# Kernel tuning notes

Measured on AMD Instinct MI355X. Metric: run time of the kernel, lower is better.

Reference implementation:

```python
import jax, jax.numpy as jnp
import numpy as np

LEVEL_SHAPES = ((100, 100), (50, 50), (25, 25))  # (H, W) per feature level
B, S, D, H, L, P, FFN = 2, 13125, 256, 8, 3, 4, 1024
Dh = D // H


def setup_inputs() -> dict:
    key = jax.random.key(0)
    ks = jax.random.split(key, 24)

    def rn(k, shape, s=0.02):
        return jax.random.normal(k, shape, jnp.float32) * s

    starts = np.cumsum([0] + [h * w for h, w in LEVEL_SHAPES])[:-1]
    return {
        "x": jax.random.normal(ks[0], (B, S, D), jnp.float32),
        "pos_embed": jax.random.normal(ks[1], (B, S, D), jnp.float32) * 0.1,
        "ref_points": jax.random.uniform(ks[2], (B, S, L, 2), jnp.float32),
        "W_off": rn(ks[3], (D, H * L * P * 2)),
        "b_off": rn(ks[4], (H * L * P * 2,), 0.5),
        "W_attn": rn(ks[5], (D, H * L * P)),
        "b_attn": rn(ks[6], (H * L * P,)),
        "W_val": rn(ks[7], (D, D)),
        "b_val": rn(ks[8], (D,)),
        "W_out": rn(ks[9], (D, D)),
        "b_out": rn(ks[10], (D,)),
        "g1": jnp.ones((D,), jnp.float32),
        "be1": jnp.zeros((D,), jnp.float32),
        "W1": rn(ks[11], (D, FFN)),
        "b1": rn(ks[12], (FFN,)),
        "W2": rn(ks[13], (FFN, D)),
        "b2": rn(ks[14], (D,)),
        "g2": jnp.ones((D,), jnp.float32),
        "be2": jnp.zeros((D,), jnp.float32),
        "level_shapes": jnp.array(LEVEL_SHAPES, jnp.int32),
        "level_start_idx": jnp.array(starts, jnp.int32),
    }


def layer_norm(x, g, b, eps=1e-5):
    m = jnp.mean(x, -1, keepdims=True)
    v = jnp.var(x, -1, keepdims=True)
    return (x - m) * jax.lax.rsqrt(v + eps) * g + b


def bilinear_sample(vl, loc, Hl, Wl):
    # vl: [B,H,S_l,Dh]; loc: [B,H,S,P,2] normalized (x,y) in [0,1]
    # grid_sample semantics: align_corners=False, padding_mode='zeros'
    x = loc[..., 0] * Wl - 0.5
    y = loc[..., 1] * Hl - 0.5
    x0 = jnp.floor(x)
    y0 = jnp.floor(y)
    fx = x - x0
    fy = y - y0
    x0i = x0.astype(jnp.int32)
    y0i = y0.astype(jnp.int32)
    out = 0.0
    for dy, dx, w in ((0, 0, (1 - fx) * (1 - fy)), (0, 1, fx * (1 - fy)),
                      (1, 0, (1 - fx) * fy), (1, 1, fx * fy)):
        xi = x0i + dx
        yi = y0i + dy
        valid = (xi >= 0) & (xi < Wl) & (yi >= 0) & (yi < Hl)
        idx = jnp.clip(yi, 0, Hl - 1) * Wl + jnp.clip(xi, 0, Wl - 1)
        b_, h_, s_, p_ = idx.shape
        g = jnp.take_along_axis(vl, idx.reshape(b_, h_, s_ * p_)[..., None], axis=2)
        g = g.reshape(b_, h_, s_, p_, Dh)
        out = out + g * (w * valid)[..., None]
    return out  # [B,H,S,P,Dh]


def ms_deform_attn(q, x, ref_points, W_off, b_off, W_attn, b_attn, W_val, b_val, W_out, b_out):
    value = (x @ W_val + b_val).reshape(B, S, H, Dh).transpose(0, 2, 1, 3)  # [B,H,S,Dh]
    off = (q @ W_off + b_off).reshape(B, S, H, L, P, 2)
    attn = jax.nn.softmax((q @ W_attn + b_attn).reshape(B, S, H, L * P), axis=-1)
    attn = attn.reshape(B, S, H, L, P).transpose(0, 2, 1, 3, 4)  # [B,H,S,L,P]
    # offset normalizer is (W, H) per level
    norm = jnp.array([[w, h] for h, w in LEVEL_SHAPES], jnp.float32)
    loc = ref_points[:, :, None, :, None, :] + off / norm[None, None, None, :, None, :]
    loc = loc.transpose(0, 2, 1, 3, 4, 5)  # [B,H,S,L,P,2]
    s0 = 0
    sampled = []
    for l, (Hl, Wl) in enumerate(LEVEL_SHAPES):
        vl = jax.lax.slice_in_dim(value, s0, s0 + Hl * Wl, axis=2)
        sampled.append(bilinear_sample(vl, loc[:, :, :, l], Hl, Wl))
        s0 += Hl * Wl
    sampled = jnp.stack(sampled, axis=3)  # [B,H,S,L,P,Dh]
    out = jnp.einsum('bhslp,bhslpd->bshd', attn, sampled).reshape(B, S, D)
    return out @ W_out + b_out


def reference(x, pos_embed, ref_points, W_off, b_off, W_attn, b_attn, W_val, b_val,
              W_out, b_out, g1, be1, W1, b1, W2, b2, g2, be2,
              level_shapes, level_start_idx):
    q = x + pos_embed
    attn_out = ms_deform_attn(q, x, ref_points, W_off, b_off, W_attn, b_attn,
                              W_val, b_val, W_out, b_out)
    h1 = layer_norm(x + attn_out, g1, be1)
    ffn = jax.nn.relu(h1 @ W1 + b1) @ W2 + b2
    return layer_norm(h1 + ffn, g2, be2)
```

## Files before the change

### kernel.cpp

```cpp
#include <hip/hip_runtime.h>
#include <hip/hip_bf16.h>

namespace {

constexpr int kB = 2, kS = 13125, kD = 256, kH = 8, kL = 3, kP = 4, kFFN = 1024, kDh = 32;
constexpr int kM = kB * kS;

typedef __attribute__((ext_vector_type(8))) short short8v;
typedef __attribute__((ext_vector_type(4))) float f32x4;
typedef __attribute__((ext_vector_type(2))) float f32x2;
typedef __attribute__((ext_vector_type(2))) unsigned int uint2v;

__device__ __forceinline__ float bf2f(unsigned short u) {
  unsigned int x = ((unsigned int)u) << 16;
  return __builtin_bit_cast(float, x);
}
__device__ __forceinline__ unsigned short f2bf(float f) {
  unsigned int u = __builtin_bit_cast(unsigned int, f);
  u += 0x7FFFu + ((u >> 16) & 1u);
  return (unsigned short)(u >> 16);
}

__device__ __forceinline__ void gload_lds16(const void* g, void* l) {
  __builtin_amdgcn_global_load_lds(
      (const __attribute__((address_space(1))) unsigned int*)g,
      (__attribute__((address_space(3))) unsigned int*)l, 16, 0, 0);
}

__global__ __launch_bounds__(256) void wprep_all(const float* __restrict__ Wv,
                                                 const float* __restrict__ Wo,
                                                 const float* __restrict__ Woff,
                                                 const float* __restrict__ Wattn,
                                                 const float* __restrict__ boff,
                                                 const float* __restrict__ battn,
                                                 const float* __restrict__ W1,
                                                 const float* __restrict__ W2,
                                                 unsigned short* __restrict__ Wvt,
                                                 unsigned short* __restrict__ Wot,
                                                 unsigned short* __restrict__ Wct,
                                                 float* __restrict__ bcomb,
                                                 unsigned short* __restrict__ W1t,
                                                 unsigned short* __restrict__ W2t) {
  int idx = blockIdx.x * 256 + threadIdx.x;
  if (idx < 65536) {
    int n = idx >> 8, k = idx & 255;
    Wvt[idx] = f2bf(Wv[k * 256 + n]);
  } else if (idx < 131072) {
    int j = idx - 65536;
    int n = j >> 8, k = j & 255;
    Wot[j] = f2bf(Wo[k * 256 + n]);
  } else if (idx < 204800) {
    int j = idx - 131072;
    int n = j >> 8, k = j & 255;
    int h = n / 36, jj = n - h * 36;
    float v = (jj < 24) ? Woff[(size_t)k * 192 + h * 24 + jj]
                        : Wattn[(size_t)k * 96 + h * 12 + (jj - 24)];
    Wct[j] = f2bf(v);
    if (j < 288) {
      int hh = j / 36, q = j - hh * 36;
      bcomb[j] = (q < 24) ? boff[hh * 24 + q] : battn[hh * 12 + (q - 24)];
    }
  } else if (idx < 466944) {
    int j = idx - 204800;
    int n = j >> 8, k = j & 255;
    W1t[j] = f2bf(W1[(size_t)k * 1024 + n]);
  } else if (idx < 729088) {
    int j = idx - 466944;
    int n = j >> 10, k = j & 1023;
    W2t[j] = f2bf(W2[(size_t)k * 256 + n]);
  }
}

__global__ __launch_bounds__(256) void prep_kernel(const float4* __restrict__ x,
                                                   const float4* __restrict__ pos,
                                                   ushort4* __restrict__ xb,
                                                   ushort4* __restrict__ qb, int n4) {
  int i = blockIdx.x * 256 + threadIdx.x;
  if (i < n4) {
    float4 a = x[i], b = pos[i];
    xb[i] = make_ushort4(f2bf(a.x), f2bf(a.y), f2bf(a.z), f2bf(a.w));
    qb[i] = make_ushort4(f2bf(a.x + b.x), f2bf(a.y + b.y),
                         f2bf(a.z + b.z), f2bf(a.w + b.w));
  }
}

template <int EPI, bool OBF, int MI, bool VHM>
__global__ __launch_bounds__(256) void mfma_gemm(const unsigned short* __restrict__ A,
                                                 const unsigned short* __restrict__ Bt,
                                                 const float* __restrict__ bias,
                                                 void* __restrict__ Cp,
                                                 int M, int N, int K) {
  constexpr int BM = MI * 32;
  __shared__ unsigned short smem[2 * 128 * 32];
  unsigned short* As = smem;
  unsigned short* Bs = smem + BM * 32;
  const int tid = threadIdx.x;
  const int w = tid >> 6, lane = tid & 63;
  const int m0 = blockIdx.y * BM, n0 = blockIdx.x * 128;
  const int wr = w >> 1, wc = w & 1;
  const int r_ = lane >> 2, sl = lane & 3;

  f32x4 acc[MI][4] = {};

  for (int k0 = 0; k0 < K; k0 += 32) {
#pragma unroll
    for (int i = 0; i < MI / 2; ++i) {
      const int row = i * 64 + w * 16 + r_;
      const int sg = sl ^ ((row >> 1) & 3);
      int arow = m0 + row;
      arow = arow < M ? arow : M - 1;
      gload_lds16(A + (size_t)arow * K + k0 + sg * 8, &As[(i * 64 + w * 16) * 32]);
    }
#pragma unroll
    for (int i = 0; i < 2; ++i) {
      const int row = i * 64 + w * 16 + r_;
      const int sg = sl ^ ((row >> 1) & 3);
      gload_lds16(Bt + (size_t)(n0 + row) * K + k0 + sg * 8, &Bs[(i * 64 + w * 16) * 32]);
    }
    __syncthreads();
    short8v a[MI], b[4];
#pragma unroll
    for (int mi = 0; mi < MI; ++mi) {
      const int row = wr * (MI * 16) + mi * 16 + (lane & 15);
      const int slot = (lane >> 4) ^ ((row >> 1) & 3);
      a[mi] = *(const short8v*)&As[row * 32 + slot * 8];
    }
#pragma unroll
    for (int ni = 0; ni < 4; ++ni) {
      const int row = wc * 64 + ni * 16 + (lane & 15);
      const int slot = (lane >> 4) ^ ((row >> 1) & 3);
      b[ni] = *(const short8v*)&Bs[row * 32 + slot * 8];
    }
#pragma unroll
    for (int mi = 0; mi < MI; ++mi)
#pragma unroll
      for (int ni = 0; ni < 4; ++ni)
        acc[mi][ni] = __builtin_amdgcn_mfma_f32_16x16x32_bf16(a[mi], b[ni], acc[mi][ni], 0, 0, 0);
    __syncthreads();
  }

  const int cr = lane >> 4, cc = lane & 15;
  if (OBF) {
    unsigned short* Cs = smem;
#pragma unroll
    for (int half = 0; half < MI / 2; ++half) {
      if (MI == 2 || wr == half) {
#pragma unroll
        for (int ni = 0; ni < 4; ++ni) {
          const int col = wc * 64 + ni * 16 + cc;
          const float bv = bias[n0 + col];
#pragma unroll
          for (int mi = 0; mi < MI; ++mi)
#pragma unroll
            for (int r = 0; r < 4; ++r) {
              const int loc = wr * (MI * 16) + mi * 16 + cr * 4 + r - half * 64;
              float v = acc[mi][ni][r] + bv;
              if (EPI == 2) v = fmaxf(v, 0.f);
              const int ch = (col >> 3) ^ (loc & 7);
              Cs[loc * 128 + ch * 8 + (col & 7)] = f2bf(v);
            }
        }
      }
      __syncthreads();
      const int lr = tid >> 4, lc = tid & 15;
#pragma unroll
      for (int pp = 0; pp < 4; ++pp) {
        const int loc = pp * 16 + lr;
        const int grow = m0 + half * 64 + loc;
        const short8v vv = *(const short8v*)&Cs[loc * 128 + ((lc ^ (loc & 7)) * 8)];
        if (grow < M) {
          if (VHM) {
            const int col = n0 + lc * 8;
            const int bb = grow >= kS ? 1 : 0;
            const int ss = grow - bb * kS;
            const int hh = col >> 5;
            *(short8v*)((unsigned short*)Cp +
                        (((size_t)(bb * kH + hh) * kS + ss) * kDh + (col & 31))) = vv;
          } else {
            *(short8v*)((unsigned short*)Cp + (size_t)grow * N + n0 + lc * 8) = vv;
          }
        }
      }
      __syncthreads();
    }
  } else {
#pragma unroll
    for (int ni = 0; ni < 4; ++ni) {
      const int col = n0 + wc * 64 + ni * 16 + cc;
      if (col >= N) continue;
      const float bv = bias[col];
#pragma unroll
      for (int mi = 0; mi < MI; ++mi) {
#pragma unroll
        for (int r = 0; r < 4; ++r) {
          const int row = m0 + wr * (MI * 16) + mi * 16 + cr * 4 + r;
          if (row >= M) continue;
          ((float*)Cp)[(size_t)row * N + col] = acc[mi][ni][r] + bv;
        }
      }
    }
  }
}

__global__ __launch_bounds__(512, 4) void ffn_fused(const unsigned short* __restrict__ Ain,
                                                    const unsigned short* __restrict__ W1t,
                                                    const unsigned short* __restrict__ W2t,
                                                    const float* __restrict__ b1,
                                                    const float* __restrict__ b2,
                                                    unsigned short* __restrict__ Cp,
                                                    int M) {
  __shared__ unsigned short W1s[2][64 * 256];
  __shared__ unsigned short Ps[2][2 * 64 * 32];
  const int tid = threadIdx.x;
  const int w = tid >> 6, lane = tid & 63;
  const int m0 = blockIdx.x * 64;
  const int cr = lane >> 4, cc = lane & 15;
  const int mw = w & 3;
  const int fw = w >> 2;

  short8v areg[8];
  {
    int grow = m0 + mw * 16 + cc;
    grow = grow < M ? grow : M - 1;
    const unsigned short* ap = Ain + (size_t)grow * 256 + cr * 8;
#pragma unroll
    for (int kk = 0; kk < 8; ++kk) areg[kk] = *(const short8v*)(ap + kk * 32);
  }

  auto stage_w1 = [&](int jt, int buf) {
    const unsigned short* src = W1t + (size_t)jt * 64 * 256;
#pragma unroll
    for (int it = 0; it < 4; ++it) {
      const int idx = it * 512 + tid;
      const int kk = idx >> 8;
      const int row = (idx >> 2) & 63;
      const int sl = idx & 3;
      const int ssl = sl ^ ((row >> 1) & 3);
      gload_lds16(src + (size_t)row * 256 + kk * 32 + ssl * 8, &W1s[buf][idx * 8]);
    }
  };

  f32x4 acc[4][2] = {};

  stage_w1(0, 0);
  __syncthreads();

#pragma unroll
  for (int jt = 0; jt < 16; ++jt) {
    const int buf = jt & 1;
    if (jt < 15) stage_w1(jt + 1, buf ^ 1);

    f32x4 p1[2] = {};
#pragma unroll
    for (int kk = 0; kk < 8; ++kk) {
#pragma unroll
      for (int lf = 0; lf < 2; ++lf) {
        const int row = fw * 32 + lf * 16 + cc;
        const short8v wv = *(const short8v*)
            &W1s[buf][kk * 2048 + row * 32 + ((cr ^ ((row >> 1) & 3)) * 8)];
        p1[lf] = __builtin_amdgcn_mfma_f32_16x16x32_bf16(wv, areg[kk], p1[lf], 0, 0, 0);
      }
    }
    {
      const int row = mw * 16 + cc;
      const int rsw = (row >> 1) & 3;
#pragma unroll
      for (int lf = 0; lf < 2; ++lf) {
        const float4 bv = *(const float4*)&b1[jt * 64 + fw * 32 + lf * 16 + cr * 4];
        const unsigned int u0 =
            (unsigned)f2bf(fmaxf(p1[lf][0] + bv.x, 0.f)) |
            ((unsigned)f2bf(fmaxf(p1[lf][1] + bv.y, 0.f)) << 16);
        const unsigned int u1 =
            (unsigned)f2bf(fmaxf(p1[lf][2] + bv.z, 0.f)) |
            ((unsigned)f2bf(fmaxf(p1[lf][3] + bv.w, 0.f)) << 16);
        const int slot = lf * 2 + (cr >> 1);
        uint2v* dst = (uint2v*)&Ps[buf][fw * 2048 + row * 32 + ((slot ^ rsw) * 8) + (cr & 1) * 4];
        *dst = (uint2v){u0, u1};
      }
    }

    if (jt > 0) {
      const unsigned short* Pr = Ps[buf ^ 1];
#pragma unroll
      for (int kk2 = 0; kk2 < 2; ++kk2) {
        short8v pf[4];
#pragma unroll
        for (int mi = 0; mi < 4; ++mi) {
          const int row = mi * 16 + cc;
          pf[mi] = *(const short8v*)
              &Pr[kk2 * 2048 + row * 32 + ((cr ^ ((row >> 1) & 3)) * 8)];
        }
#pragma unroll
        for (int ni = 0; ni < 2; ++ni) {
          const int ncol = w * 32 + ni * 16 + cc;
          const short8v wv = *(const short8v*)
              (W2t + (size_t)ncol * 1024 + (jt - 1) * 64 + kk2 * 32 + cr * 8);
#pragma unroll
          for (int mi = 0; mi < 4; ++mi)
            acc[mi][ni] = __builtin_amdgcn_mfma_f32_16x16x32_bf16(pf[mi], wv, acc[mi][ni], 0, 0, 0);
        }
      }
    }
    __syncthreads();
  }

  {
    const unsigned short* Pr = Ps[1];
#pragma unroll
    for (int kk2 = 0; kk2 < 2; ++kk2) {
      short8v pf[4];
#pragma unroll
      for (int mi = 0; mi < 4; ++mi) {
        const int row = mi * 16 + cc;
        pf[mi] = *(const short8v*)
            &Pr[kk2 * 2048 + row * 32 + ((cr ^ ((row >> 1) & 3)) * 8)];
      }
#pragma unroll
      for (int ni = 0; ni < 2; ++ni) {
        const int ncol = w * 32 + ni * 16 + cc;
        const short8v wv = *(const short8v*)
            (W2t + (size_t)ncol * 1024 + 15 * 64 + kk2 * 32 + cr * 8);
#pragma unroll
        for (int mi = 0; mi < 4; ++mi)
          acc[mi][ni] = __builtin_amdgcn_mfma_f32_16x16x32_bf16(pf[mi], wv, acc[mi][ni], 0, 0, 0);
      }
    }
  }
  __syncthreads();

  unsigned short* Cs = &W1s[0][0];
#pragma unroll
  for (int ni = 0; ni < 2; ++ni) {
    const int col = w * 32 + ni * 16 + cc;
    const float bv = b2[col];
#pragma unroll
    for (int mi = 0; mi < 4; ++mi)
#pragma unroll
      for (int r = 0; r < 4; ++r) {
        const int row = mi * 16 + cr * 4 + r;
        const float v = acc[mi][ni][r] + bv;
        Cs[row * 256 + (((col >> 3) ^ (row & 7)) * 8) + (col & 7)] = f2bf(v);
      }
  }
  __syncthreads();
#pragma unroll
  for (int it = 0; it < 4; ++it) {
    const int row = it * 16 + (tid >> 5);
    const int grow = m0 + row;
    const int ch = tid & 31;
    const short8v vv = *(const short8v*)&Cs[row * 256 + ((ch ^ (row & 7)) * 8)];
    if (grow < M) *(short8v*)(Cp + (size_t)grow * 256 + ch * 8) = vv;
  }
}

__device__ __forceinline__ void acc2u(f32x2* acc, unsigned u, int i, float m) {
  f32x2 v;
  v.x = __builtin_bit_cast(float, u << 16);
  v.y = __builtin_bit_cast(float, u & 0xFFFF0000u);
  acc[i] += m * v;
}
__device__ __forceinline__ void acc_corner(f32x2* acc, uint4 q, float m) {
  acc2u(acc, q.x, 0, m);
  acc2u(acc, q.y, 1, m);
  acc2u(acc, q.z, 2, m);
  acc2u(acc, q.w, 3, m);
}

__global__ __launch_bounds__(256) void sample_kernel(const unsigned short* __restrict__ value,
                                                     const float* __restrict__ oa,
                                                     const float* __restrict__ refp,
                                                     unsigned short* __restrict__ out) {
  const int tid = threadIdx.x;
  const int sub = tid >> 2;
  const int lane = tid & 3;
  const int gi = blockIdx.x * 64 + sub;
  if (gi >= kB * kS * kH) return;
  const int h = gi & 7;
  const int bs = gi >> 3;
  const int b = (bs >= kS) ? 1 : 0;

  const float* op = oa + (size_t)bs * 288 + h * 36;
  const float* al = op + 24;
  float w[12];
  float mx = -1e30f;
#pragma unroll
  for (int i = 0; i < 12; ++i) { w[i] = al[i]; mx = fmaxf(mx, w[i]); }
  float sum = 0.f;
#pragma unroll
  for (int i = 0; i < 12; ++i) { w[i] = __expf(w[i] - mx); sum += w[i]; }
  const float inv = 1.f / sum;
#pragma unroll
  for (int i = 0; i < 12; ++i) w[i] *= inv;

  const float* rp = refp + (size_t)bs * (kL * 2);
  const unsigned short* vbase = value + ((size_t)(b * kH + h) * kS) * kDh + lane * 8;

  const int LH[3] = {100, 50, 25}, LW[3] = {100, 50, 25}, LS[3] = {0, 10000, 12500};
  f32x2 acc[4] = {};
#pragma unroll
  for (int l = 0; l < 3; ++l) {
    const int Wi = LW[l], Hi = LH[l];
    const float Wl = (float)Wi, Hl = (float)Hi;
    const float rxw = rp[l * 2 + 0] * Wl - 0.5f;
    const float ryh = rp[l * 2 + 1] * Hl - 0.5f;
    const unsigned short* lvl = vbase + (size_t)LS[l] * kDh;
#pragma unroll
    for (int p = 0; p < 4; ++p) {
      const float ox = op[l * 8 + p * 2 + 0], oy = op[l * 8 + p * 2 + 1];
      const float xf = rxw + ox;
      const float yf = ryh + oy;
      const float x0f = floorf(xf), y0f = floorf(yf);
      const float fx = xf - x0f, fy = yf - y0f;
      const int x0 = (int)x0f, y0 = (int)y0f;
      const int x1 = x0 + 1, y1 = y0 + 1;
      const bool vx0 = (unsigned)x0 < (unsigned)Wi;
      const bool vx1 = (unsigned)x1 < (unsigned)Wi;
      const bool vy0 = (unsigned)y0 < (unsigned)Hi;
      const bool vy1 = (unsigned)y1 < (unsigned)Hi;
      const int cx0 = min(max(x0, 0), Wi - 1), cx1 = min(max(x1, 0), Wi - 1);
      const int cy0 = min(max(y0, 0), Hi - 1), cy1 = min(max(y1, 0), Hi - 1);
      const float aw = w[l * 4 + p];
      const float ax = aw * fx, a0 = aw - ax;
      const float w00 = a0 - a0 * fy, w10 = a0 * fy;
      const float w01 = ax - ax * fy, w11 = ax * fy;
      const float m00 = (vx0 && vy0) ? w00 : 0.f;
      const float m01 = (vx1 && vy0) ? w01 : 0.f;
      const float m10 = (vx0 && vy1) ? w10 : 0.f;
      const float m11 = (vx1 && vy1) ? w11 : 0.f;
      const int ry0 = cy0 * Wi, ry1 = cy1 * Wi;
      const uint4 q00 = *(const uint4*)(lvl + (size_t)(ry0 + cx0) * kDh);
      const uint4 q01 = *(const uint4*)(lvl + (size_t)(ry0 + cx1) * kDh);
      const uint4 q10 = *(const uint4*)(lvl + (size_t)(ry1 + cx0) * kDh);
      const uint4 q11 = *(const uint4*)(lvl + (size_t)(ry1 + cx1) * kDh);
      acc_corner(acc, q00, m00);
      acc_corner(acc, q01, m01);
      acc_corner(acc, q10, m10);
      acc_corner(acc, q11, m11);
    }
  }
  unsigned short r[8];
#pragma unroll
  for (int i = 0; i < 4; ++i) {
    r[2 * i] = f2bf(acc[i].x);
    r[2 * i + 1] = f2bf(acc[i].y);
  }
  *(short8v*)(out + (size_t)bs * kD + h * kDh + lane * 8) = *(const short8v*)r;
}

template <int WB>
__global__ __launch_bounds__(256) void lnres_kernel(const float* __restrict__ X,
                                                    const unsigned short* __restrict__ Ab,
                                                    const float* __restrict__ g,
                                                    const float* __restrict__ be,
                                                    float* __restrict__ out,
                                                    unsigned short* __restrict__ outb,
                                                    int rows) {
  const int wid = threadIdx.x >> 6, lane = threadIdx.x & 63;
  const int row = blockIdx.x * 4 + wid;
  if (row >= rows) return;
  const float4 v = ((const float4*)(X + (size_t)row * kD))[lane];
  const ushort4 a4 = ((const ushort4*)(Ab + (size_t)row * kD))[lane];
  float4 t;
  t.x = v.x + bf2f(a4.x);
  t.y = v.y + bf2f(a4.y);
  t.z = v.z + bf2f(a4.z);
  t.w = v.w + bf2f(a4.w);
  float s = t.x + t.y + t.z + t.w;
  float sq = t.x * t.x + t.y * t.y + t.z * t.z + t.w * t.w;
#pragma unroll
  for (int o = 1; o < 64; o <<= 1) {
    s += __shfl_xor(s, o);
    sq += __shfl_xor(sq, o);
  }
  const float mean = s * (1.f / kD);
  const float var = sq * (1.f / kD) - mean * mean;
  const float rs = rsqrtf(var + 1e-5f);
  const float4 gg = ((const float4*)g)[lane];
  const float4 bb = ((const float4*)be)[lane];
  float4 o4;
  o4.x = (t.x - mean) * rs * gg.x + bb.x;
  o4.y = (t.y - mean) * rs * gg.y + bb.y;
  o4.z = (t.z - mean) * rs * gg.z + bb.z;
  o4.w = (t.w - mean) * rs * gg.w + bb.w;
  ((float4*)(out + (size_t)row * kD))[lane] = o4;
  if (WB) {
    ((ushort4*)(outb + (size_t)row * kD))[lane] =
        make_ushort4(f2bf(o4.x), f2bf(o4.y), f2bf(o4.z), f2bf(o4.w));
  }
}

}

extern "C" void kernel_launch(void* const* d_in, const int* in_sizes, int n_in,
                              void* d_out, int out_size, void* d_ws, size_t ws_size,
                              hipStream_t stream) {
  const float* x      = (const float*)d_in[0];
  const float* pos    = (const float*)d_in[1];
  const float* refp   = (const float*)d_in[2];
  const float* W_off  = (const float*)d_in[3];
  const float* b_off  = (const float*)d_in[4];
  const float* W_attn = (const float*)d_in[5];
  const float* b_attn = (const float*)d_in[6];
  const float* W_val  = (const float*)d_in[7];
  const float* b_val  = (const float*)d_in[8];
  const float* W_out  = (const float*)d_in[9];
  const float* b_out  = (const float*)d_in[10];
  const float* g1     = (const float*)d_in[11];
  const float* be1    = (const float*)d_in[12];
  const float* W1     = (const float*)d_in[13];
  const float* b1     = (const float*)d_in[14];
  const float* W2     = (const float*)d_in[15];
  const float* b2     = (const float*)d_in[16];
  const float* g2     = (const float*)d_in[17];
  const float* be2    = (const float*)d_in[18];
  float* outp = (float*)d_out;

  char* ws = (char*)d_ws;
  unsigned short* Wvt = (unsigned short*)(ws + 0);
  unsigned short* Wot = (unsigned short*)(ws + 131072);
  unsigned short* Wct = (unsigned short*)(ws + 262144);
  float* bcomb        = (float*)(ws + 262144 + 288 * 512);
  unsigned short* W1t = (unsigned short*)(ws + 458752);
  unsigned short* W2t = (unsigned short*)(ws + 983040);
  const size_t MDb = (size_t)kM * kD * 2;
  char* regA = ws + 1507328;
  char* regB = regA + MDb;
  char* regC = regB + MDb;
  char* regG = regC + 43680000;

  unsigned short* xb    = (unsigned short*)regA;
  unsigned short* aob   = (unsigned short*)regA;
  unsigned short* qb    = (unsigned short*)regB;
  unsigned short* f2b   = (unsigned short*)regB;
  unsigned short* value = (unsigned short*)regC;
  float* oa   = (float*)(regC + MDb);
  float* h1   = (float*)regC;
  unsigned short* h1b = (unsigned short*)(regC + (size_t)kM * kD * 4);
  unsigned short* sv  = (unsigned short*)regG;

  const dim3 blk(256);
  const int mt64 = (kM + 63) / 64;
  const int n4 = kM * kD / 4;

  wprep_all<<<(729088 + 255) / 256, blk, 0, stream>>>(W_val, W_out, W_off, W_attn,
                                                      b_off, b_attn, W1, W2,
                                                      Wvt, Wot, Wct, bcomb, W1t, W2t);
  prep_kernel<<<(n4 + 255) / 256, blk, 0, stream>>>((const float4*)x, (const float4*)pos,
                                                    (ushort4*)xb, (ushort4*)qb, n4);
  mfma_gemm<0, true, 2, true><<<dim3(2, mt64), blk, 0, stream>>>(xb, Wvt, b_val, value,
                                                                 kM, 256, 256);
  mfma_gemm<0, false, 2, false><<<dim3(3, mt64), blk, 0, stream>>>(qb, Wct, bcomb, oa,
                                                                   kM, 288, 256);
  sample_kernel<<<(kB * kS * kH + 63) / 64, blk, 0, stream>>>(value, oa, refp, sv);
  mfma_gemm<0, true, 2, false><<<dim3(2, mt64), blk, 0, stream>>>(sv, Wot, b_out, aob,
                                                                  kM, 256, 256);
  lnres_kernel<1><<<(kM + 3) / 4, blk, 0, stream>>>(x, aob, g1, be1, h1, h1b, kM);
  ffn_fused<<<mt64, dim3(512), 0, stream>>>(h1b, W1t, W2t, b1, b2, f2b, kM);
  lnres_kernel<0><<<(kM + 3) / 4, blk, 0, stream>>>(h1, f2b, g2, be2, outp, nullptr, kM);
}
```

Before: 197.2 us.

## Restructure fused FFN: single P buffer, shared W1 fragment across two row tiles

The fused FFN kernel now has each wave compute a 16-column hidden slice for two 16-row tiles, so every W1 fragment read from LDS feeds two MFMAs. The ReLU'd hidden tile goes into a single 64x64 LDS buffer with a new XOR swizzle, and the second GEMM runs in the same iteration instead of one step behind. This halves LDS reads of W1 and shrinks the P buffer. In exchange it adds a second __syncthreads per iteration, drops the full unroll of the outer loop, and doubles the register-held A fragments.

```diff
diff --git a/kernel.cpp b/kernel.cpp
--- a/kernel.cpp
+++ b/kernel.cpp
@@ -210,21 +210,22 @@
                                                     unsigned short* __restrict__ Cp,
                                                     int M) {
   __shared__ unsigned short W1s[2][64 * 256];
-  __shared__ unsigned short Ps[2][2 * 64 * 32];
+  __shared__ unsigned short Ps[64 * 64];
   const int tid = threadIdx.x;
   const int w = tid >> 6, lane = tid & 63;
   const int m0 = blockIdx.x * 64;
   const int cr = lane >> 4, cc = lane & 15;
-  const int mw = w & 3;
-  const int fw = w >> 2;
-
-  short8v areg[8];
-  {
-    int grow = m0 + mw * 16 + cc;
+  const int fq = w & 3;
+  const int mh = w >> 2;
+
+  short8v areg[2][8];
+#pragma unroll
+  for (int mi = 0; mi < 2; ++mi) {
+    int grow = m0 + (mh * 2 + mi) * 16 + cc;
     grow = grow < M ? grow : M - 1;
     const unsigned short* ap = Ain + (size_t)grow * 256 + cr * 8;
 #pragma unroll
-    for (int kk = 0; kk < 8; ++kk) areg[kk] = *(const short8v*)(ap + kk * 32);
+    for (int kk = 0; kk < 8; ++kk) areg[mi][kk] = *(const short8v*)(ap + kk * 32);
   }
 
   auto stage_w1 = [&](int jt, int buf) {
@@ -245,88 +246,61 @@
   stage_w1(0, 0);
   __syncthreads();
 
-#pragma unroll
   for (int jt = 0; jt < 16; ++jt) {
     const int buf = jt & 1;
     if (jt < 15) stage_w1(jt + 1, buf ^ 1);
 
     f32x4 p1[2] = {};
-#pragma unroll
-    for (int kk = 0; kk < 8; ++kk) {
-#pragma unroll
-      for (int lf = 0; lf < 2; ++lf) {
-        const int row = fw * 32 + lf * 16 + cc;
+    {
+      const int row = fq * 16 + cc;
+      const int rsw = (row >> 1) & 3;
+#pragma unroll
+      for (int kk = 0; kk < 8; ++kk) {
         const short8v wv = *(const short8v*)
-            &W1s[buf][kk * 2048 + row * 32 + ((cr ^ ((row >> 1) & 3)) * 8)];
-        p1[lf] = __builtin_amdgcn_mfma_f32_16x16x32_bf16(wv, areg[kk], p1[lf], 0, 0, 0);
+            &W1s[buf][kk * 2048 + row * 32 + ((cr ^ rsw) * 8)];
+        p1[0] = __builtin_amdgcn_mfma_f32_16x16x32_bf16(wv, areg[0][kk], p1[0], 0, 0, 0);
+        p1[1] = __builtin_amdgcn_mfma_f32_16x16x32_bf16(wv, areg[1][kk], p1[1], 0, 0, 0);
       }
     }
     {
-      const int row = mw * 16 + cc;
-      const int rsw = (row >> 1) & 3;
-#pragma unroll
-      for (int lf = 0; lf < 2; ++lf) {
-        const float4 bv = *(const float4*)&b1[jt * 64 + fw * 32 + lf * 16 + cr * 4];
+      const float4 bv = *(const float4*)&b1[jt * 64 + fq * 16 + cr * 4];
+#pragma unroll
+      for (int mi = 0; mi < 2; ++mi) {
+        const int mrow = (mh * 2 + mi) * 16 + cc;
         const unsigned int u0 =
-            (unsigned)f2bf(fmaxf(p1[lf][0] + bv.x, 0.f)) |
-            ((unsigned)f2bf(fmaxf(p1[lf][1] + bv.y, 0.f)) << 16);
+            (unsigned)f2bf(fmaxf(p1[mi][0] + bv.x, 0.f)) |
+            ((unsigned)f2bf(fmaxf(p1[mi][1] + bv.y, 0.f)) << 16);
         const unsigned int u1 =
-            (unsigned)f2bf(fmaxf(p1[lf][2] + bv.z, 0.f)) |
-            ((unsigned)f2bf(fmaxf(p1[lf][3] + bv.w, 0.f)) << 16);
-        const int slot = lf * 2 + (cr >> 1);
-        uint2v* dst = (uint2v*)&Ps[buf][fw * 2048 + row * 32 + ((slot ^ rsw) * 8) + (cr & 1) * 4];
+            (unsigned)f2bf(fmaxf(p1[mi][2] + bv.z, 0.f)) |
+            ((unsigned)f2bf(fmaxf(p1[mi][3] + bv.w, 0.f)) << 16);
+        const int slot = (fq * 4 + cr) ^ ((mrow & 7) << 1);
+        uint2v* dst = (uint2v*)&Ps[mrow * 64 + slot * 4];
         *dst = (uint2v){u0, u1};
       }
     }
-
-    if (jt > 0) {
-      const unsigned short* Pr = Ps[buf ^ 1];
-#pragma unroll
-      for (int kk2 = 0; kk2 < 2; ++kk2) {
-        short8v pf[4];
-#pragma unroll
-        for (int mi = 0; mi < 4; ++mi) {
-          const int row = mi * 16 + cc;
-          pf[mi] = *(const short8v*)
-              &Pr[kk2 * 2048 + row * 32 + ((cr ^ ((row >> 1) & 3)) * 8)];
-        }
-#pragma unroll
-        for (int ni = 0; ni < 2; ++ni) {
-          const int ncol = w * 32 + ni * 16 + cc;
-          const short8v wv = *(const short8v*)
-              (W2t + (size_t)ncol * 1024 + (jt - 1) * 64 + kk2 * 32 + cr * 8);
-#pragma unroll
-          for (int mi = 0; mi < 4; ++mi)
-            acc[mi][ni] = __builtin_amdgcn_mfma_f32_16x16x32_bf16(pf[mi], wv, acc[mi][ni], 0, 0, 0);
-        }
-      }
-    }
     __syncthreads();
-  }
-
-  {
-    const unsigned short* Pr = Ps[1];
+
 #pragma unroll
     for (int kk2 = 0; kk2 < 2; ++kk2) {
       short8v pf[4];
 #pragma unroll
       for (int mi = 0; mi < 4; ++mi) {
-        const int row = mi * 16 + cc;
-        pf[mi] = *(const short8v*)
-            &Pr[kk2 * 2048 + row * 32 + ((cr ^ ((row >> 1) & 3)) * 8)];
+        const int mrow = mi * 16 + cc;
+        const int slot = (kk2 * 8 + cr * 2) ^ ((mrow & 7) << 1);
+        pf[mi] = *(const short8v*)&Ps[mrow * 64 + slot * 4];
       }
 #pragma unroll
       for (int ni = 0; ni < 2; ++ni) {
         const int ncol = w * 32 + ni * 16 + cc;
-        const short8v wv = *(const short8v*)
-            (W2t + (size_t)ncol * 1024 + 15 * 64 + kk2 * 32 + cr * 8);
+        const short8v wv =
+            *(const short8v*)(W2t + (size_t)ncol * 1024 + jt * 64 + kk2 * 32 + cr * 8);
 #pragma unroll
         for (int mi = 0; mi < 4; ++mi)
           acc[mi][ni] = __builtin_amdgcn_mfma_f32_16x16x32_bf16(pf[mi], wv, acc[mi][ni], 0, 0, 0);
       }
     }
-  }
-  __syncthreads();
+    __syncthreads();
+  }
 
   unsigned short* Cs = &W1s[0][0];
 #pragma unroll
```

New measurement: 244.7 us. +24.0%, slower.
